# Kernel optimization log

Hardware: AMD Instinct MI355X
Metric: run time of the kernel (lower is better)

## Reference

```python
import jax, jax.numpy as jnp
import numpy as np

N = 100000   # nodes
E = 1600000  # edges
D = 128      # in_dim
H = 128      # hidden_dim
C = 40       # num_classes
EPS = 1e-5   # LayerNorm eps (torch default)


def setup_inputs() -> dict:
    key = jax.random.key(0)
    ks = jax.random.split(key, 16)
    x = jax.random.normal(ks[0], (N, D), dtype=jnp.float32)
    edge_index = jax.random.randint(ks[1], (2, E), 0, N, dtype=jnp.int64)
    s = 1.0 / np.sqrt(D)
    inp = {"x": x, "edge_index": edge_index}
    # 3 GCN layers: weight [in, H], bias [H]; LayerNorm gamma/beta [H]
    for i in range(3):
        inp[f"W{i}"] = jax.random.normal(ks[2 + i], (D if i == 0 else H, H), dtype=jnp.float32) * s
        inp[f"b{i}"] = jnp.zeros((H,), jnp.float32)
        inp[f"g{i}"] = jnp.ones((H,), jnp.float32)
        inp[f"be{i}"] = jnp.zeros((H,), jnp.float32)
    inp["Wc"] = jax.random.normal(ks[10], (H, C), dtype=jnp.float32) * (1.0 / np.sqrt(H))
    inp["bc"] = jnp.zeros((C,), jnp.float32)
    return inp


def _layer_norm(h, g, b):
    mu = jnp.mean(h, axis=-1, keepdims=True)
    var = jnp.var(h, axis=-1, keepdims=True)  # biased, matches torch
    return (h - mu) * jax.lax.rsqrt(var + EPS) * g + b


def _gcn_conv(x, W, b, src, dst, enorm, dinv2):
    # GCNConv: D^{-1/2}(A+I)D^{-1/2} X W + b (self-loops handled analytically)
    h = x @ W                                   # [N, H]
    agg = jax.ops.segment_sum(h[src] * enorm[:, None], dst, num_segments=N)
    return agg + h * dinv2[:, None] + b


def reference(x, edge_index, W0, b0, g0, be0, W1, b1, g1, be1, W2, b2, g2, be2, Wc, bc):
    src, dst = edge_index[0], edge_index[1]
    # degree with self-loops (GCNConv adds self-loops by default)
    deg = jnp.zeros((N,), x.dtype).at[dst].add(1.0) + 1.0
    dinv = jax.lax.rsqrt(deg)
    enorm = dinv[src] * dinv[dst]               # per-edge normalization
    dinv2 = dinv * dinv                         # self-loop normalization

    Ws, bs, gs, bes = (W0, W1, W2), (b0, b1, b2), (g0, g1, g2), (be0, be1, be2)
    for i in range(3):
        x_in = x
        x = _gcn_conv(x, Ws[i], bs[i], src, dst, enorm, dinv2)
        x = _layer_norm(x, gs[i], bes[i])
        x = jax.nn.elu(x)
        if i > 0:
            x = x + x_in
        # dropout: eval mode / p=0 -> identity
    return x @ Wc + bc
```

## Files before the change

### kernel.cpp

```cpp
#include <hip/hip_runtime.h>
#include <math.h>

#define N_NODES 100000
#define N_EDGES 1600000
#define DIM     128
#define NCLS    40
#define NBUCK   196
#define P1_CH   4096
#define P1_GRID 391

typedef _Float16 f16x8 __attribute__((ext_vector_type(8)));
typedef _Float16 f16x2 __attribute__((ext_vector_type(2)));
typedef float    f32x4 __attribute__((ext_vector_type(4)));

__device__ inline unsigned short f16bits(float f) {
    union { _Float16 h; unsigned short u; } cv;
    cv.h = (_Float16)f;
    return cv.u;
}
__device__ inline f16x2 as_h2(unsigned u) {
    union { unsigned u; f16x2 h; } cv;
    cv.u = u;
    return cv.h;
}
__device__ inline unsigned as_u(f16x2 h) {
    union { f16x2 h; unsigned u; } cv;
    cv.h = h;
    return cv.u;
}
__device__ inline unsigned pack_h2(float lo, float hi) {
    f16x2 h;
    h.x = (_Float16)lo;
    h.y = (_Float16)hi;
    return as_u(h);
}
__device__ inline int wave_incl_scan(int v, int lane) {
#pragma unroll
    for (int off = 1; off < 64; off <<= 1) {
        int x = __shfl_up(v, off, 64);
        if (lane >= off) v += x;
    }
    return v;
}

__global__ __launch_bounds__(256) void setup_misc(const float* __restrict__ W0,
                                                  const float* __restrict__ W1,
                                                  const float* __restrict__ W2,
                                                  const float* __restrict__ Wc,
                                                  const int* __restrict__ ei,
                                                  unsigned short* __restrict__ Wsw0,
                                                  unsigned short* __restrict__ Wsw1,
                                                  unsigned short* __restrict__ Wsw2,
                                                  unsigned short* __restrict__ Wcsw,
                                                  int* __restrict__ bcnt) {
    int blk = blockIdx.x;
    if (blk < 192) {
        const float* W = (blk < 64) ? W0 : (blk < 128) ? W1 : W2;
        unsigned short* Wsw = (blk < 64) ? Wsw0 : (blk < 128) ? Wsw1 : Wsw2;
        int o = (blk & 63) * 256 + threadIdx.x;
        int f = o >> 9;
        int l = (o >> 3) & 63;
        int j = o & 7;
        int n = f >> 2;
        int s = f & 3;
        int k = s * 32 + (l >> 4) * 8 + j;
        int c = (l & 15) * 8 + n;
        Wsw[o] = f16bits(W[k * DIM + c]);
    } else if (blk < 216) {
        int o = (blk - 192) * 256 + threadIdx.x;
        int f = o >> 9;
        int l = (o >> 3) & 63;
        int j = o & 7;
        int n = f >> 2;
        int s = f & 3;
        int k = s * 32 + (l >> 4) * 8 + j;
        int c = (l & 15) * 3 + n;
        Wcsw[o] = (c < NCLS) ? f16bits(Wc[k * NCLS + c]) : (unsigned short)0;
    } else {
        __shared__ int h[256];
        const int t  = threadIdx.x;
        const int e0 = (blk - 216) * P1_CH;
        const int cnt = min(P1_CH, N_EDGES - e0);
        h[t] = 0;
        __syncthreads();
        for (int i = t; i < cnt; i += 256)
            atomicAdd(&h[ei[N_EDGES + e0 + i] >> 9], 1);
        __syncthreads();
        if (h[t]) atomicAdd(&bcnt[t], h[t]);
    }
}

__global__ __launch_bounds__(256) void bscan(const int* __restrict__ bcnt,
                                             int* __restrict__ bbase,
                                             int* __restrict__ bcur) {
    __shared__ int wtot[4];
    int t = threadIdx.x;
    int lane = t & 63, wv = t >> 6;
    int v = (t < NBUCK) ? bcnt[t] : 0;
    int incl = wave_incl_scan(v, lane);
    if (lane == 63) wtot[wv] = incl;
    __syncthreads();
    int prefix = 0;
    for (int i = 0; i < wv; ++i) prefix += wtot[i];
    incl += prefix;
    int excl = incl - v;
    if (t < NBUCK) {
        bbase[t] = excl;
        bcur[t]  = excl;
    }
    if (t == 0) bbase[NBUCK] = N_EDGES;
}

__global__ __launch_bounds__(256) void bucket_p1(const int* __restrict__ ei,
                                                 int* __restrict__ bcur,
                                                 unsigned* __restrict__ tmp) {
    __shared__ int  hist[256];
    __shared__ int  lscan[256];
    __shared__ int  rank[256];
    __shared__ int  gbase[256];
    __shared__ int  wtot[4];
    __shared__ int2 stage[P1_CH];
    const int t  = threadIdx.x;
    const int lane = t & 63, wv = t >> 6;
    const int e0 = blockIdx.x * P1_CH;
    const int cnt = min(P1_CH, N_EDGES - e0);

    hist[t] = 0;
    __syncthreads();

    int2 ed[16];
#pragma unroll
    for (int i = 0; i < 16; ++i) {
        int idx = t + i * 256;
        if (idx < cnt) {
            int s = ei[e0 + idx];
            int d = ei[N_EDGES + e0 + idx];
            ed[i] = make_int2(s, d);
            atomicAdd(&hist[d >> 9], 1);
        }
    }
    __syncthreads();

    int hv = hist[t];
    int incl = wave_incl_scan(hv, lane);
    if (lane == 63) wtot[wv] = incl;
    __syncthreads();
    int prefix = 0;
    for (int i = 0; i < wv; ++i) prefix += wtot[i];
    incl += prefix;
    int excl = incl - hv;
    lscan[t] = excl;
    rank[t]  = excl;
    if (hv > 0) gbase[t] = atomicAdd(&bcur[t], hv);
    __syncthreads();

#pragma unroll
    for (int i = 0; i < 16; ++i) {
        int idx = t + i * 256;
        if (idx < cnt) {
            int b = ed[i].y >> 9;
            int p = atomicAdd(&rank[b], 1);
            stage[p] = ed[i];
        }
    }
    __syncthreads();

    for (int p = t; p < cnt; p += 256) {
        int2 v = stage[p];
        int b = v.y >> 9;
        tmp[gbase[b] + (p - lscan[b])] = ((unsigned)v.x << 9) | ((unsigned)v.y & 511u);
    }
}

__global__ __launch_bounds__(256) void bucket_p2(const unsigned* __restrict__ tmp,
                                                 const int* __restrict__ bbase,
                                                 int* __restrict__ rowptr,
                                                 float* __restrict__ dinv,
                                                 unsigned* __restrict__ rec) {
    __shared__ int cnt[512];
    __shared__ int cur[512];
    __shared__ int wtot[4];
    const int t  = threadIdx.x;
    const int lane = t & 63, wv = t >> 6;
    const int b  = blockIdx.x;
    const int d0 = b << 9;
    const int dend = min(d0 + 512, N_NODES);
    const int nn = dend - d0;

    cnt[t] = 0;
    cnt[t + 256] = 0;
    __syncthreads();

    const int beg = bbase[b];
    const int end = bbase[b + 1];
    for (int idx = beg + t; idx < end; idx += 256)
        atomicAdd(&cnt[tmp[idx] & 511u], 1);
    __syncthreads();

    int c0 = cnt[2 * t];
    int c1 = cnt[2 * t + 1];
    int pv = c0 + c1;
    int incl = wave_incl_scan(pv, lane);
    if (lane == 63) wtot[wv] = incl;
    __syncthreads();
    int prefix = 0;
    for (int i = 0; i < wv; ++i) prefix += wtot[i];
    incl += prefix;
    int excl = incl - pv;
    int base0 = beg + excl;
    int base1 = base0 + c0;
    cur[2 * t]     = base0;
    cur[2 * t + 1] = base1;
    if (2 * t < nn) {
        rowptr[d0 + 2 * t] = base0;
        dinv[d0 + 2 * t]   = rsqrtf((float)c0 + 1.0f);
    }
    if (2 * t + 1 < nn) {
        rowptr[d0 + 2 * t + 1] = base1;
        dinv[d0 + 2 * t + 1]   = rsqrtf((float)c1 + 1.0f);
    }
    if (b == NBUCK - 1 && t == 0) rowptr[N_NODES] = N_EDGES;
    __syncthreads();

    for (int idx = beg + t; idx < end; idx += 256) {
        unsigned u = tmp[idx];
        int pos = atomicAdd(&cur[u & 511u], 1);
        rec[pos] = (u >> 9) << 8;
    }
}

__global__ __launch_bounds__(256) void gemm_mfma_f(const float* __restrict__ X,
                                                   const unsigned short* __restrict__ Wsw,
                                                   const float* __restrict__ dinv,
                                                   unsigned short* __restrict__ H) {
    __shared__ unsigned short wlds[32 * 512];
    const int tid   = threadIdx.x;
    const int lane  = tid & 63;
    const int wave  = tid >> 6;
    const int row0w = blockIdx.x * 64 + wave * 16;
    const int m = lane & 15;
    const int q = lane >> 4;

    {
        const uint4* srcp = (const uint4*)Wsw;
        uint4*       dstp = (uint4*)wlds;
#pragma unroll
        for (int i = 0; i < 8; ++i) dstp[tid + i * 256] = srcp[tid + i * 256];
    }
    __syncthreads();

    int r = row0w + m;
    if (r >= N_NODES) r = N_NODES - 1;
    const float* xp = X + (size_t)r * DIM + q * 8;
    f16x8 af[4];
#pragma unroll
    for (int s = 0; s < 4; ++s) {
        float4 x0 = *(const float4*)(xp + s * 32);
        float4 x1 = *(const float4*)(xp + s * 32 + 4);
        f16x8 v;
        v[0] = (_Float16)x0.x; v[1] = (_Float16)x0.y;
        v[2] = (_Float16)x0.z; v[3] = (_Float16)x0.w;
        v[4] = (_Float16)x1.x; v[5] = (_Float16)x1.y;
        v[6] = (_Float16)x1.z; v[7] = (_Float16)x1.w;
        af[s] = v;
    }

    f32x4 acc[8];
    f32x4 z = {0.f, 0.f, 0.f, 0.f};
#pragma unroll
    for (int n = 0; n < 8; ++n) acc[n] = z;

    const unsigned short* wl = wlds + lane * 8;
#pragma unroll
    for (int s = 0; s < 4; ++s)
#pragma unroll
        for (int n = 0; n < 8; ++n) {
            f16x8 wf = *(const f16x8*)(wl + ((n * 4 + s) << 9));
            acc[n] = __builtin_amdgcn_mfma_f32_16x16x32_f16(af[s], wf, acc[n], 0, 0, 0);
        }

#pragma unroll
    for (int j = 0; j < 4; ++j) {
        int row = row0w + q * 4 + j;
        if (row < N_NODES) {
            float dv = dinv[row];
            uint4 o;
            o.x = pack_h2(acc[0][j] * dv, acc[1][j] * dv);
            o.y = pack_h2(acc[2][j] * dv, acc[3][j] * dv);
            o.z = pack_h2(acc[4][j] * dv, acc[5][j] * dv);
            o.w = pack_h2(acc[6][j] * dv, acc[7][j] * dv);
            *(uint4*)(H + (size_t)row * DIM + m * 8) = o;
        } else {
            uint4 zz = make_uint4(0u, 0u, 0u, 0u);
            *(uint4*)(H + (size_t)row * DIM + m * 8) = zz;
        }
    }
}

__global__ __launch_bounds__(256) void gemm_mfma_h(const unsigned short* __restrict__ Xh,
                                                   const unsigned short* __restrict__ Wsw,
                                                   const float* __restrict__ dinv,
                                                   unsigned short* __restrict__ H) {
    __shared__ unsigned short wlds[32 * 512];
    const int tid   = threadIdx.x;
    const int lane  = tid & 63;
    const int wave  = tid >> 6;
    const int row0w = blockIdx.x * 64 + wave * 16;
    const int m = lane & 15;
    const int q = lane >> 4;

    {
        const uint4* srcp = (const uint4*)Wsw;
        uint4*       dstp = (uint4*)wlds;
#pragma unroll
        for (int i = 0; i < 8; ++i) dstp[tid + i * 256] = srcp[tid + i * 256];
    }
    __syncthreads();

    int r = row0w + m;
    if (r >= N_NODES) r = N_NODES - 1;
    const unsigned short* xp = Xh + (size_t)r * DIM + q * 8;
    f16x8 af[4];
#pragma unroll
    for (int s = 0; s < 4; ++s) af[s] = *(const f16x8*)(xp + s * 32);

    f32x4 acc[8];
    f32x4 z = {0.f, 0.f, 0.f, 0.f};
#pragma unroll
    for (int n = 0; n < 8; ++n) acc[n] = z;

    const unsigned short* wl = wlds + lane * 8;
#pragma unroll
    for (int s = 0; s < 4; ++s)
#pragma unroll
        for (int n = 0; n < 8; ++n) {
            f16x8 wf = *(const f16x8*)(wl + ((n * 4 + s) << 9));
            acc[n] = __builtin_amdgcn_mfma_f32_16x16x32_f16(af[s], wf, acc[n], 0, 0, 0);
        }

#pragma unroll
    for (int j = 0; j < 4; ++j) {
        int row = row0w + q * 4 + j;
        if (row < N_NODES) {
            float dv = dinv[row];
            uint4 o;
            o.x = pack_h2(acc[0][j] * dv, acc[1][j] * dv);
            o.y = pack_h2(acc[2][j] * dv, acc[3][j] * dv);
            o.z = pack_h2(acc[4][j] * dv, acc[5][j] * dv);
            o.w = pack_h2(acc[6][j] * dv, acc[7][j] * dv);
            *(uint4*)(H + (size_t)row * DIM + m * 8) = o;
        } else {
            uint4 zz = make_uint4(0u, 0u, 0u, 0u);
            *(uint4*)(H + (size_t)row * DIM + m * 8) = zz;
        }
    }
}

__global__ __launch_bounds__(256) void agg_ln(const unsigned short* __restrict__ Hh,
                                              const unsigned short* __restrict__ xin,
                                              const float* __restrict__ dinv,
                                              const float* __restrict__ bias,
                                              const float* __restrict__ g,
                                              const float* __restrict__ be,
                                              const int* __restrict__ rowptr,
                                              const unsigned* __restrict__ rec,
                                              unsigned short* __restrict__ outb) {
    int node = blockIdx.x * 4 + (threadIdx.x >> 6);
    int lane = threadIdx.x & 63;
    int sub  = lane & 15;
    int qtr  = lane >> 4;
    int beg = rowptr[node];
    int end = rowptr[node + 1];
    const char* Hb8 = (const char*)Hh;
    const unsigned laneoff = (unsigned)sub * 16;
    const unsigned sentin  = (unsigned)N_NODES << 8;

    f16x2 acc[4];
    f16x2 hz = {(_Float16)0.f, (_Float16)0.f};
#pragma unroll
    for (int k = 0; k < 4; ++k) acc[k] = hz;

    for (int e0 = beg; e0 < end; e0 += 64) {
        int cnt = min(end - e0, 64);
        unsigned sv = (lane < cnt) ? rec[e0 + lane] : sentin;
        int cntR = (cnt + 15) & ~15;
        for (int j = 0; j < cntR; j += 16) {
            unsigned o0 = (unsigned)__shfl((int)sv, j + qtr, 64) + laneoff;
            unsigned o1 = (unsigned)__shfl((int)sv, j + 4 + qtr, 64) + laneoff;
            unsigned o2 = (unsigned)__shfl((int)sv, j + 8 + qtr, 64) + laneoff;
            unsigned o3 = (unsigned)__shfl((int)sv, j + 12 + qtr, 64) + laneoff;
            uint4 u0 = *(const uint4*)(Hb8 + o0);
            uint4 u1 = *(const uint4*)(Hb8 + o1);
            uint4 u2 = *(const uint4*)(Hb8 + o2);
            uint4 u3 = *(const uint4*)(Hb8 + o3);
            acc[0] += as_h2(u0.x);
            acc[1] += as_h2(u0.y);
            acc[2] += as_h2(u0.z);
            acc[3] += as_h2(u0.w);
            acc[0] += as_h2(u1.x);
            acc[1] += as_h2(u1.y);
            acc[2] += as_h2(u1.z);
            acc[3] += as_h2(u1.w);
            acc[0] += as_h2(u2.x);
            acc[1] += as_h2(u2.y);
            acc[2] += as_h2(u2.z);
            acc[3] += as_h2(u2.w);
            acc[0] += as_h2(u3.x);
            acc[1] += as_h2(u3.y);
            acc[2] += as_h2(u3.z);
            acc[3] += as_h2(u3.w);
        }
    }

#pragma unroll
    for (int k = 0; k < 4; ++k) {
        acc[k] += as_h2(__shfl_xor(as_u(acc[k]), 16, 64));
        acc[k] += as_h2(__shfl_xor(as_u(acc[k]), 32, 64));
    }

    unsigned mu = as_u(acc[0]);
    mu = (qtr == 1) ? as_u(acc[1]) : mu;
    mu = (qtr == 2) ? as_u(acc[2]) : mu;
    mu = (qtr == 3) ? as_u(acc[3]) : mu;
    f16x2 mine = as_h2(mu);
    const int c0 = sub * 8 + qtr * 2;
    const unsigned nodeoff = ((unsigned)node << 8) + (unsigned)c0 * 2;

    float dv = dinv[node];
    f16x2 hh = as_h2(*(const unsigned*)(Hb8 + nodeoff));
    float2 bb = *(const float2*)(bias + c0);
    float a0 = ((float)mine.x + (float)hh.x) * dv + bb.x;
    float a1 = ((float)mine.y + (float)hh.y) * dv + bb.y;

    float s1 = a0 + a1;
    float s2 = a0 * a0 + a1 * a1;
#pragma unroll
    for (int mk = 1; mk <= 32; mk <<= 1) {
        s1 += __shfl_xor(s1, mk, 64);
        s2 += __shfl_xor(s2, mk, 64);
    }
    float mean = s1 * (1.0f / 128.0f);
    float var  = s2 * (1.0f / 128.0f) - mean * mean;
    float rr   = rsqrtf(var + 1e-5f);
    float2 gg = *(const float2*)(g + c0);
    float2 ee = *(const float2*)(be + c0);
    float r0 = (a0 - mean) * rr * gg.x + ee.x;
    float r1 = (a1 - mean) * rr * gg.y + ee.y;
    r0 = r0 > 0.0f ? r0 : expm1f(r0);
    r1 = r1 > 0.0f ? r1 : expm1f(r1);
    if (xin) {
        f16x2 xi = as_h2(*(const unsigned*)((const char*)xin + nodeoff));
        r0 += (float)xi.x;
        r1 += (float)xi.y;
    }
    *(unsigned*)((char*)outb + nodeoff) = pack_h2(r0, r1);
}

__global__ __launch_bounds__(256) void classifier_mfma(const unsigned short* __restrict__ Xh,
                                                       const unsigned short* __restrict__ Wcsw,
                                                       const float* __restrict__ bc,
                                                       float* __restrict__ out) {
    __shared__ unsigned short wlds[12 * 512];
    const int tid   = threadIdx.x;
    const int lane  = tid & 63;
    const int wave  = tid >> 6;
    const int row0w = blockIdx.x * 128 + wave * 32;
    const int m = lane & 15;
    const int q = lane >> 4;

    {
        const uint4* srcp = (const uint4*)Wcsw;
        uint4*       dstp = (uint4*)wlds;
#pragma unroll
        for (int i = 0; i < 3; ++i) dstp[tid + i * 256] = srcp[tid + i * 256];
    }
    __syncthreads();

    f16x8 wf[12];
#pragma unroll
    for (int f = 0; f < 12; ++f)
        wf[f] = *(const f16x8*)(wlds + (f << 9) + lane * 8);

    f16x8 af[2][4];
#pragma unroll
    for (int ggr = 0; ggr < 2; ++ggr) {
        int r = row0w + ggr * 16 + m;
        if (r >= N_NODES) r = N_NODES - 1;
        const unsigned short* xp = Xh + (size_t)r * DIM + q * 8;
#pragma unroll
        for (int s = 0; s < 4; ++s) af[ggr][s] = *(const f16x8*)(xp + s * 32);
    }

    f32x4 acc[2][3];
    f32x4 z = {0.f, 0.f, 0.f, 0.f};
#pragma unroll
    for (int ggr = 0; ggr < 2; ++ggr)
#pragma unroll
        for (int n = 0; n < 3; ++n) acc[ggr][n] = z;

#pragma unroll
    for (int s = 0; s < 4; ++s)
#pragma unroll
        for (int n = 0; n < 3; ++n) {
            acc[0][n] = __builtin_amdgcn_mfma_f32_16x16x32_f16(af[0][s], wf[n * 4 + s], acc[0][n], 0, 0, 0);
            acc[1][n] = __builtin_amdgcn_mfma_f32_16x16x32_f16(af[1][s], wf[n * 4 + s], acc[1][n], 0, 0, 0);
        }

    float bcv[3];
#pragma unroll
    for (int n = 0; n < 3; ++n) {
        int c = 3 * m + n;
        bcv[n] = (c < NCLS) ? bc[c] : 0.f;
    }

#pragma unroll
    for (int ggr = 0; ggr < 2; ++ggr)
#pragma unroll
        for (int j = 0; j < 4; ++j) {
            int row = row0w + ggr * 16 + q * 4 + j;
            if (row < N_NODES) {
#pragma unroll
                for (int n = 0; n < 3; ++n) {
                    int c = 3 * m + n;
                    if (c < NCLS)
                        out[(size_t)row * NCLS + c] = acc[ggr][n][j] + bcv[n];
                }
            }
        }
}

extern "C" void kernel_launch(void* const* d_in, const int* in_sizes, int n_in,
                              void* d_out, int out_size, void* d_ws, size_t ws_size,
                              hipStream_t stream) {
    const float* x  = (const float*)d_in[0];
    const int*   ei = (const int*)d_in[1];
    const float* W[3]  = {(const float*)d_in[2], (const float*)d_in[6], (const float*)d_in[10]};
    const float* b[3]  = {(const float*)d_in[3], (const float*)d_in[7], (const float*)d_in[11]};
    const float* g[3]  = {(const float*)d_in[4], (const float*)d_in[8], (const float*)d_in[12]};
    const float* be[3] = {(const float*)d_in[5], (const float*)d_in[9], (const float*)d_in[13]};
    const float* Wc = (const float*)d_in[14];
    const float* bc = (const float*)d_in[15];
    float* out = (float*)d_out;

    char* ws = (char*)d_ws;
    const size_t NP = 400128;
    float* dinv   = (float*)(ws);
    int*   rowptr = (int*)  (ws + NP);
    int*   bcnt   = (int*)  (ws + 2 * NP);
    int*   bbase  = (int*)  (ws + 2 * NP + 1024);
    int*   bcur   = (int*)  (ws + 2 * NP + 2048);
    unsigned* rec = (unsigned*)(ws + 2 * NP + 4096);
    unsigned short* Hh = (unsigned short*)(ws + 2 * NP + 4096 + (size_t)N_EDGES * 8);
    unsigned short* Ah = Hh + (size_t)(N_NODES + 64) * DIM;
    unsigned short* Ch = Ah + (size_t)N_NODES * DIM;
    unsigned short* Wsw0 = Ch + (size_t)N_NODES * DIM;
    unsigned short* Wsw1 = Wsw0 + DIM * DIM;
    unsigned short* Wsw2 = Wsw1 + DIM * DIM;
    unsigned short* Wcsw = Wsw2 + DIM * DIM;
    unsigned* tmp = (unsigned*)Ch;

    hipMemsetAsync(bcnt, 0, 1024, stream);
    setup_misc<<<216 + P1_GRID, 256, 0, stream>>>(W[0], W[1], W[2], Wc, ei,
                                                  Wsw0, Wsw1, Wsw2, Wcsw, bcnt);

    bscan<<<1, 256, 0, stream>>>(bcnt, bbase, bcur);
    bucket_p1<<<P1_GRID, 256, 0, stream>>>(ei, bcur, tmp);
    bucket_p2<<<NBUCK, 256, 0, stream>>>(tmp, bbase, rowptr, dinv, rec);

    const int gemm_grid = (N_NODES + 63) / 64;
    const int cls_grid  = (N_NODES + 127) / 128;
    const int agg_grid  = N_NODES / 4;

    gemm_mfma_f<<<gemm_grid, 256, 0, stream>>>(x, Wsw0, dinv, Hh);
    agg_ln<<<agg_grid, 256, 0, stream>>>(Hh, nullptr, dinv, b[0], g[0], be[0], rowptr, rec, Ch);

    gemm_mfma_h<<<gemm_grid, 256, 0, stream>>>(Ch, Wsw1, dinv, Hh);
    agg_ln<<<agg_grid, 256, 0, stream>>>(Hh, Ch, dinv, b[1], g[1], be[1], rowptr, rec, Ah);

    gemm_mfma_h<<<gemm_grid, 256, 0, stream>>>(Ah, Wsw2, dinv, Hh);
    agg_ln<<<agg_grid, 256, 0, stream>>>(Hh, Ah, dinv, b[2], g[2], be[2], rowptr, rec, Ch);

    classifier_mfma<<<cls_grid, 256, 0, stream>>>(Ch, Wcsw, bc, out);
}
```

Measured before the change: 410.9 us.

## Map one node per 16-lane group in aggregation kernel, 8 gathers in flight

The aggregation+LayerNorm kernel now assigns each node to a 16-lane group (16 nodes per block) instead of a full 64-lane wave. Each lane owns 8 contiguous features, walks the node's edges itself, and keeps 8 row gathers in flight with four independent accumulator sets. This drops the cross-quarter shuffle reduction and shortens the LayerNorm reduction to 4 steps. The aim is less wasted lane work on low-degree nodes and more memory-level parallelism, at the cost of more registers and possible load imbalance between groups in a wave.

```diff
diff --git a/kernel.cpp b/kernel.cpp
--- a/kernel.cpp
+++ b/kernel.cpp
@@ -365,95 +365,119 @@
                                               const int* __restrict__ rowptr,
                                               const unsigned* __restrict__ rec,
                                               unsigned short* __restrict__ outb) {
-    int node = blockIdx.x * 4 + (threadIdx.x >> 6);
-    int lane = threadIdx.x & 63;
-    int sub  = lane & 15;
-    int qtr  = lane >> 4;
-    int beg = rowptr[node];
-    int end = rowptr[node + 1];
+    const int tid  = threadIdx.x;
+    const int lane = tid & 63;
+    const int l16  = tid & 15;
+    const int gb   = lane & 48;
+    const int node = blockIdx.x * 16 + (tid >> 4);
+    const int beg  = rowptr[node];
+    const int end  = rowptr[node + 1];
     const char* Hb8 = (const char*)Hh;
-    const unsigned laneoff = (unsigned)sub * 16;
+    const unsigned laneoff = (unsigned)l16 * 16;
     const unsigned sentin  = (unsigned)N_NODES << 8;
 
-    f16x2 acc[4];
+    f16x2 accA[4], accB[4], accC[4], accD[4];
     f16x2 hz = {(_Float16)0.f, (_Float16)0.f};
 #pragma unroll
-    for (int k = 0; k < 4; ++k) acc[k] = hz;
-
-    for (int e0 = beg; e0 < end; e0 += 64) {
-        int cnt = min(end - e0, 64);
-        unsigned sv = (lane < cnt) ? rec[e0 + lane] : sentin;
-        int cntR = (cnt + 15) & ~15;
-        for (int j = 0; j < cntR; j += 16) {
-            unsigned o0 = (unsigned)__shfl((int)sv, j + qtr, 64) + laneoff;
-            unsigned o1 = (unsigned)__shfl((int)sv, j + 4 + qtr, 64) + laneoff;
-            unsigned o2 = (unsigned)__shfl((int)sv, j + 8 + qtr, 64) + laneoff;
-            unsigned o3 = (unsigned)__shfl((int)sv, j + 12 + qtr, 64) + laneoff;
+    for (int k = 0; k < 4; ++k) { accA[k] = hz; accB[k] = hz; accC[k] = hz; accD[k] = hz; }
+
+    for (int e0 = beg; e0 < end; e0 += 16) {
+        int cnt = min(end - e0, 16);
+        unsigned sv = (l16 < cnt) ? rec[e0 + l16] : sentin;
+        int cntR = (cnt + 7) & ~7;
+        for (int j = 0; j < cntR; j += 8) {
+            unsigned o0 = (unsigned)__shfl((int)sv, gb + j + 0, 64) + laneoff;
+            unsigned o1 = (unsigned)__shfl((int)sv, gb + j + 1, 64) + laneoff;
+            unsigned o2 = (unsigned)__shfl((int)sv, gb + j + 2, 64) + laneoff;
+            unsigned o3 = (unsigned)__shfl((int)sv, gb + j + 3, 64) + laneoff;
+            unsigned o4 = (unsigned)__shfl((int)sv, gb + j + 4, 64) + laneoff;
+            unsigned o5 = (unsigned)__shfl((int)sv, gb + j + 5, 64) + laneoff;
+            unsigned o6 = (unsigned)__shfl((int)sv, gb + j + 6, 64) + laneoff;
+            unsigned o7 = (unsigned)__shfl((int)sv, gb + j + 7, 64) + laneoff;
             uint4 u0 = *(const uint4*)(Hb8 + o0);
             uint4 u1 = *(const uint4*)(Hb8 + o1);
             uint4 u2 = *(const uint4*)(Hb8 + o2);
             uint4 u3 = *(const uint4*)(Hb8 + o3);
-            acc[0] += as_h2(u0.x);
-            acc[1] += as_h2(u0.y);
-            acc[2] += as_h2(u0.z);
-            acc[3] += as_h2(u0.w);
-            acc[0] += as_h2(u1.x);
-            acc[1] += as_h2(u1.y);
-            acc[2] += as_h2(u1.z);
-            acc[3] += as_h2(u1.w);
-            acc[0] += as_h2(u2.x);
-            acc[1] += as_h2(u2.y);
-            acc[2] += as_h2(u2.z);
-            acc[3] += as_h2(u2.w);
-            acc[0] += as_h2(u3.x);
-            acc[1] += as_h2(u3.y);
-            acc[2] += as_h2(u3.z);
-            acc[3] += as_h2(u3.w);
-        }
-    }
-
-#pragma unroll
-    for (int k = 0; k < 4; ++k) {
-        acc[k] += as_h2(__shfl_xor(as_u(acc[k]), 16, 64));
-        acc[k] += as_h2(__shfl_xor(as_u(acc[k]), 32, 64));
-    }
-
-    unsigned mu = as_u(acc[0]);
-    mu = (qtr == 1) ? as_u(acc[1]) : mu;
-    mu = (qtr == 2) ? as_u(acc[2]) : mu;
-    mu = (qtr == 3) ? as_u(acc[3]) : mu;
-    f16x2 mine = as_h2(mu);
-    const int c0 = sub * 8 + qtr * 2;
-    const unsigned nodeoff = ((unsigned)node << 8) + (unsigned)c0 * 2;
-
-    float dv = dinv[node];
-    f16x2 hh = as_h2(*(const unsigned*)(Hb8 + nodeoff));
-    float2 bb = *(const float2*)(bias + c0);
-    float a0 = ((float)mine.x + (float)hh.x) * dv + bb.x;
-    float a1 = ((float)mine.y + (float)hh.y) * dv + bb.y;
-
-    float s1 = a0 + a1;
-    float s2 = a0 * a0 + a1 * a1;
-#pragma unroll
-    for (int mk = 1; mk <= 32; mk <<= 1) {
+            uint4 u4 = *(const uint4*)(Hb8 + o4);
+            uint4 u5 = *(const uint4*)(Hb8 + o5);
+            uint4 u6 = *(const uint4*)(Hb8 + o6);
+            uint4 u7 = *(const uint4*)(Hb8 + o7);
+            accA[0] += as_h2(u0.x); accA[1] += as_h2(u0.y); accA[2] += as_h2(u0.z); accA[3] += as_h2(u0.w);
+            accB[0] += as_h2(u1.x); accB[1] += as_h2(u1.y); accB[2] += as_h2(u1.z); accB[3] += as_h2(u1.w);
+            accC[0] += as_h2(u2.x); accC[1] += as_h2(u2.y); accC[2] += as_h2(u2.z); accC[3] += as_h2(u2.w);
+            accD[0] += as_h2(u3.x); accD[1] += as_h2(u3.y); accD[2] += as_h2(u3.z); accD[3] += as_h2(u3.w);
+            accA[0] += as_h2(u4.x); accA[1] += as_h2(u4.y); accA[2] += as_h2(u4.z); accA[3] += as_h2(u4.w);
+            accB[0] += as_h2(u5.x); accB[1] += as_h2(u5.y); accB[2] += as_h2(u5.z); accB[3] += as_h2(u5.w);
+            accC[0] += as_h2(u6.x); accC[1] += as_h2(u6.y); accC[2] += as_h2(u6.z); accC[3] += as_h2(u6.w);
+            accD[0] += as_h2(u7.x); accD[1] += as_h2(u7.y); accD[2] += as_h2(u7.z); accD[3] += as_h2(u7.w);
+        }
+    }
+
+#pragma unroll
+    for (int k = 0; k < 4; ++k) accA[k] = (accA[k] + accB[k]) + (accC[k] + accD[k]);
+
+    const float dv = dinv[node];
+    const unsigned nodeoff = ((unsigned)node << 8) + laneoff;
+    uint4 hv = *(const uint4*)(Hb8 + nodeoff);
+    const int c0 = l16 * 8;
+    float4 bb0 = *(const float4*)(bias + c0);
+    float4 bb1 = *(const float4*)(bias + c0 + 4);
+    f16x2 h0 = as_h2(hv.x), h1 = as_h2(hv.y), h2 = as_h2(hv.z), h3 = as_h2(hv.w);
+
+    float a[8];
+    a[0] = ((float)accA[0].x + (float)h0.x) * dv + bb0.x;
+    a[1] = ((float)accA[0].y + (float)h0.y) * dv + bb0.y;
+    a[2] = ((float)accA[1].x + (float)h1.x) * dv + bb0.z;
+    a[3] = ((float)accA[1].y + (float)h1.y) * dv + bb0.w;
+    a[4] = ((float)accA[2].x + (float)h2.x) * dv + bb1.x;
+    a[5] = ((float)accA[2].y + (float)h2.y) * dv + bb1.y;
+    a[6] = ((float)accA[3].x + (float)h3.x) * dv + bb1.z;
+    a[7] = ((float)accA[3].y + (float)h3.y) * dv + bb1.w;
+
+    float s1 = 0.f, s2 = 0.f;
+#pragma unroll
+    for (int i = 0; i < 8; ++i) { s1 += a[i]; s2 += a[i] * a[i]; }
+#pragma unroll
+    for (int mk = 1; mk <= 8; mk <<= 1) {
         s1 += __shfl_xor(s1, mk, 64);
         s2 += __shfl_xor(s2, mk, 64);
     }
     float mean = s1 * (1.0f / 128.0f);
     float var  = s2 * (1.0f / 128.0f) - mean * mean;
     float rr   = rsqrtf(var + 1e-5f);
-    float2 gg = *(const float2*)(g + c0);
-    float2 ee = *(const float2*)(be + c0);
-    float r0 = (a0 - mean) * rr * gg.x + ee.x;
-    float r1 = (a1 - mean) * rr * gg.y + ee.y;
-    r0 = r0 > 0.0f ? r0 : expm1f(r0);
-    r1 = r1 > 0.0f ? r1 : expm1f(r1);
+
+    float4 gg0 = *(const float4*)(g + c0);
+    float4 gg1 = *(const float4*)(g + c0 + 4);
+    float4 ee0 = *(const float4*)(be + c0);
+    float4 ee1 = *(const float4*)(be + c0 + 4);
+
+    float r[8];
+    r[0] = (a[0] - mean) * rr * gg0.x + ee0.x;
+    r[1] = (a[1] - mean) * rr * gg0.y + ee0.y;
+    r[2] = (a[2] - mean) * rr * gg0.z + ee0.z;
+    r[3] = (a[3] - mean) * rr * gg0.w + ee0.w;
+    r[4] = (a[4] - mean) * rr * gg1.x + ee1.x;
+    r[5] = (a[5] - mean) * rr * gg1.y + ee1.y;
+    r[6] = (a[6] - mean) * rr * gg1.z + ee1.z;
+    r[7] = (a[7] - mean) * rr * gg1.w + ee1.w;
+#pragma unroll
+    for (int i = 0; i < 8; ++i) r[i] = r[i] > 0.0f ? r[i] : expm1f(r[i]);
+
     if (xin) {
-        f16x2 xi = as_h2(*(const unsigned*)((const char*)xin + nodeoff));
-        r0 += (float)xi.x;
-        r1 += (float)xi.y;
-    }
-    *(unsigned*)((char*)outb + nodeoff) = pack_h2(r0, r1);
+        uint4 xv = *(const uint4*)((const char*)xin + nodeoff);
+        f16x2 x0 = as_h2(xv.x), x1 = as_h2(xv.y), x2 = as_h2(xv.z), x3 = as_h2(xv.w);
+        r[0] += (float)x0.x; r[1] += (float)x0.y;
+        r[2] += (float)x1.x; r[3] += (float)x1.y;
+        r[4] += (float)x2.x; r[5] += (float)x2.y;
+        r[6] += (float)x3.x; r[7] += (float)x3.y;
+    }
+
+    uint4 o;
+    o.x = pack_h2(r[0], r[1]);
+    o.y = pack_h2(r[2], r[3]);
+    o.z = pack_h2(r[4], r[5]);
+    o.w = pack_h2(r[6], r[7]);
+    *(uint4*)((char*)outb + nodeoff) = o;
 }
 
 __global__ __launch_bounds__(256) void classifier_mfma(const unsigned short* __restrict__ Xh,
@@ -569,7 +593,7 @@
 
     const int gemm_grid = (N_NODES + 63) / 64;
     const int cls_grid  = (N_NODES + 127) / 128;
-    const int agg_grid  = N_NODES / 4;
+    const int agg_grid  = N_NODES / 16;
 
     gemm_mfma_f<<<gemm_grid, 256, 0, stream>>>(x, Wsw0, dinv, Hh);
     agg_ln<<<agg_grid, 256, 0, stream>>>(Hh, nullptr, dinv, b[0], g[0], be[0], rowptr, rec, Ch);
```

Result: faster. 401.5 us (-2.3%).
